# Optimization experiments

Measured on AMD Instinct MI355X. Metric: run time of the kernel, lower is better.

The kernel has to match this reference:

```python
import jax, jax.numpy as jnp
import numpy as np
from jax import lax

B, T, H, L, LAT, OUT, NH = 4096, 60, 512, 2, 128, 14, 4
EPS = 1e-5


def _ln(x, g, b):
    m = x.mean(-1, keepdims=True)
    v = ((x - m) ** 2).mean(-1, keepdims=True)
    return (x - m) / jnp.sqrt(v + EPS) * g + b


def setup_inputs() -> dict:
    key = jax.random.key(0)
    ks = jax.random.split(key, 24)
    f32 = jnp.float32
    def rn(k, shape, s=0.05):
        return jax.random.normal(k, shape, dtype=f32) * s
    return {
        'x': jax.random.normal(ks[0], (B, T, 17), dtype=f32),
        'conv1_w': rn(ks[1], (24, 9, 3)), 'conv1_b': rn(ks[2], (24,)),
        'bn1_g': jnp.ones(24, f32), 'bn1_b': jnp.zeros(24, f32),
        'bn1_rm': rn(ks[3], (24,), 0.1), 'bn1_rv': jnp.full((24,), 0.8, f32),
        'comp_w': rn(ks[4], (20, 8)), 'comp_b': rn(ks[5], (20,)),
        'proj_w': rn(ks[6], (H, 44)), 'proj_b': rn(ks[7], (H,)),
        'gates_w': rn(ks[8], (L, 5, H, 2 * H), 0.02), 'gates_b': rn(ks[9], (L, 5, H)),
        'retention': jnp.full((L, H), 0.9, f32),
        'expln_g': jnp.ones((L, H), f32), 'expln_b': jnp.zeros((L, H), f32),
        'ln_g': jnp.ones((L, H), f32), 'ln_b': jnp.zeros((L, H), f32),
        'attn_in_w': rn(ks[10], (3 * H, H), 0.02), 'attn_in_b': rn(ks[11], (3 * H,)),
        'attn_out_w': rn(ks[12], (H, H), 0.02), 'attn_out_b': rn(ks[13], (H,)),
        'bneck_w': rn(ks[14], (LAT, H)), 'bneck_b': rn(ks[15], (LAT,)),
        'bn2_g': jnp.ones(LAT, f32), 'bn2_b': jnp.zeros(LAT, f32),
        'bn2_rm': rn(ks[16], (LAT,), 0.1), 'bn2_rv': jnp.full((LAT,), 0.9, f32),
        'out_w': rn(ks[17], (OUT, LAT)), 'out_b': rn(ks[18], (OUT,)),
    }


def _forward(x, conv1_w, conv1_b, bn1_g, bn1_b, bn1_rm, bn1_rv, comp_w, comp_b,
             proj_w, proj_b, gates_w, gates_b, retention, expln_g, expln_b,
             ln_g, ln_b, attn_in_w, attn_in_b, attn_out_w, attn_out_b,
             bneck_w, bneck_b, bn2_g, bn2_b, bn2_rm, bn2_rv, out_w, out_b):
    bsz = x.shape[0]
    hd = proj_w.shape[0]
    nlayers = gates_w.shape[0]
    # --- conv branch on relative features (eval-mode BatchNorm) ---
    rel = x[:, :, :9].transpose(0, 2, 1)                      # [B,9,T]
    y = lax.conv_general_dilated(rel, conv1_w, (1,), [(1, 1)],
                                 dimension_numbers=('NCH', 'OIH', 'NCH'))
    y = jax.nn.relu(y + conv1_b[None, :, None])
    y = (y - bn1_rm[None, :, None]) / jnp.sqrt(bn1_rv + EPS)[None, :, None] \
        * bn1_g[None, :, None] + bn1_b[None, :, None]
    th = y.shape[2] // 2
    y = y[:, :, :th * 2].reshape(bsz, 24, th, 2).max(-1)      # MaxPool1d(2)
    rel_feat = y.transpose(0, 2, 1)                           # [B,30,24]
    # --- company embedding branch ---
    comp = jax.nn.relu(x[:, :30, 9:] @ comp_w.T + comp_b)     # [B,30,20]
    combined = jnp.concatenate([rel_feat, comp], -1) @ proj_w.T + proj_b  # [B,30,H]
    # --- stacked xLSTM over time ---
    h0 = jnp.zeros((nlayers, bsz, hd), x.dtype)
    c0 = jnp.zeros((nlayers, bsz, hd), x.dtype)
    def step(carry, x_t):
        h, c = carry
        inp = x_t
        hs, cs = [], []
        for l in range(nlayers):
            comb = jnp.concatenate([inp, h[l]], -1)           # [B,2H]
            g = jnp.einsum('bk,ghk->gbh', comb, gates_w[l]) + gates_b[l][:, None, :]
            f = jax.nn.sigmoid(g[0]); i = jax.nn.sigmoid(g[1])
            o = jax.nn.sigmoid(g[2]); cc = jnp.tanh(g[3]); m = jax.nn.sigmoid(g[4])
            r = retention[l]
            c_new = f * c[l] + i * cc
            c_new = c_new * r + (1 - r) * c[l]
            c_new = m * c_new + (1 - m) * c[l]
            o_exp = jax.nn.sigmoid(_ln(o, expln_g[l], expln_b[l]))  # exp(z)/(1+exp(z))
            h_new = _ln(o_exp * jnp.tanh(c_new), ln_g[l], ln_b[l])
            hs.append(h_new); cs.append(c_new)
            inp = h_new
        return (jnp.stack(hs), jnp.stack(cs)), inp
    _, seq = lax.scan(step, (h0, c0), combined.transpose(1, 0, 2))
    seq = seq.transpose(1, 0, 2)                              # [B,30,H]
    # --- multi-head self attention (eval, 4 heads) ---
    dh = hd // NH
    qkv = seq @ attn_in_w.T + attn_in_b
    q, k, v = jnp.split(qkv, 3, axis=-1)
    q = q.reshape(bsz, -1, NH, dh); k = k.reshape(bsz, -1, NH, dh); v = v.reshape(bsz, -1, NH, dh)
    scores = jnp.einsum('bqhd,bkhd->bhqk', q, k) / jnp.sqrt(jnp.float32(dh))
    attn = jnp.einsum('bhqk,bkhd->bqhd', jax.nn.softmax(scores, -1), v)
    attn = attn.reshape(bsz, -1, hd) @ attn_out_w.T + attn_out_b
    final = attn[:, -1, :]
    latent = final @ bneck_w.T + bneck_b
    latent = (latent - bn2_rm) / jnp.sqrt(bn2_rv + EPS) * bn2_g + bn2_b
    return latent @ out_w.T + out_b


def reference(x, conv1_w, conv1_b, bn1_g, bn1_b, bn1_rm, bn1_rv, comp_w, comp_b,
              proj_w, proj_b, gates_w, gates_b, retention, expln_g, expln_b,
              ln_g, ln_b, attn_in_w, attn_in_b, attn_out_w, attn_out_b,
              bneck_w, bneck_b, bn2_g, bn2_b, bn2_rm, bn2_rv, out_w, out_b):
    return _forward(x, conv1_w, conv1_b, bn1_g, bn1_b, bn1_rm, bn1_rv, comp_w, comp_b,
                    proj_w, proj_b, gates_w, gates_b, retention, expln_g, expln_b,
                    ln_g, ln_b, attn_in_w, attn_in_b, attn_out_w, attn_out_b,
                    bneck_w, bneck_b, bn2_g, bn2_b, bn2_rm, bn2_rv, out_w, out_b)
```

## Files before the change

kernel.cpp:

```cpp
#include <hip/hip_runtime.h>
#include <hip/hip_bf16.h>

#define B_   4096
#define T_   60
#define TT   30
#define H_   512
#define L_   2
#define NH_  4
#define DH_  128
#define LAT_ 128
#define OUT_ 14
#define NGATE_ (5*H_)
#define EPSF 1e-5f
#define FEATK 64
#define K0M  (FEATK + H_)

typedef __attribute__((ext_vector_type(8))) short bf16x8;
typedef __attribute__((ext_vector_type(4))) float f32x4;

__device__ __forceinline__ float sigmoidf_(float x) { return 1.0f / (1.0f + __expf(-x)); }
__device__ __forceinline__ float bf2f(short s) {
    return __uint_as_float(((unsigned)(unsigned short)s) << 16);
}

__device__ __forceinline__ void async_load16(const void* g, void* l) {
    __builtin_amdgcn_global_load_lds((const __attribute__((address_space(1))) void*)g,
                                     (__attribute__((address_space(3))) void*)l, 16, 0, 0);
}

__global__ __launch_bounds__(256) void cvt_bf16(const float* __restrict__ in,
                                                __hip_bfloat16* __restrict__ out, long n) {
    long i = (long)blockIdx.x * blockDim.x + threadIdx.x;
    long stride = (long)gridDim.x * blockDim.x;
    for (; i < n; i += stride) out[i] = __float2bfloat16(in[i]);
}

__global__ __launch_bounds__(256) void zero_f32(float* __restrict__ p, long n) {
    long i = (long)blockIdx.x * blockDim.x + threadIdx.x;
    long stride = (long)gridDim.x * blockDim.x;
    for (; i < n; i += stride) p[i] = 0.0f;
}

__global__ __launch_bounds__(256)
void build_w0m(const float* __restrict__ gw, const float* __restrict__ pw,
               const float* __restrict__ pb, const float* __restrict__ gb,
               __hip_bfloat16* __restrict__ w0m, float* __restrict__ bc) {
    const int tid = threadIdx.x;
    const int n = blockIdx.x * 4 + (tid >> 6);
    const int f = tid & 63;
    const float* wrow = gw + (long)n * (2 * H_);
    float acc = 0.f;
    if (f < 44) {
        for (int k = 0; k < H_; ++k) acc += wrow[k] * pw[k * 44 + f];
    }
    w0m[(long)n * K0M + f] = __float2bfloat16(acc);
    #pragma unroll
    for (int j = 0; j < 8; ++j) {
        int col = f * 8 + j;
        w0m[(long)n * K0M + FEATK + col] = __float2bfloat16(wrow[H_ + col]);
    }
    float s = 0.f;
    #pragma unroll
    for (int j = 0; j < 8; ++j) s += wrow[f * 8 + j] * pb[f * 8 + j];
    #pragma unroll
    for (int off = 32; off > 0; off >>= 1) s += __shfl_down(s, off, 64);
    if (f == 0) bc[n] = gb[n] + s;
}

__global__ __launch_bounds__(256)
void build_wkd(const float* __restrict__ aiw, __hip_bfloat16* __restrict__ wkd) {
    int i = blockIdx.x * 256 + threadIdx.x;
    if (i >= 2048 * 512) return;
    int n = i >> 9, k = i & 511;
    float v = ((k >> 7) == (n >> 9)) ? aiw[(H_ + k) * H_ + (n & 511)] : 0.f;
    wkd[i] = __float2bfloat16(v);
}

__global__ __launch_bounds__(256)
void build_wvd(const float* __restrict__ aiw, __hip_bfloat16* __restrict__ wvd) {
    int i = blockIdx.x * 256 + threadIdx.x;
    if (i >= 512 * 2048) return;
    int n = i >> 11, k = i & 2047;
    float v = ((k >> 9) == (n >> 7)) ? aiw[(2 * H_ + n) * H_ + (k & 511)] : 0.f;
    wvd[i] = __float2bfloat16(v);
}

__global__ __launch_bounds__(256)
void frontend_kernel(const float* __restrict__ x,
                     const float* __restrict__ cw, const float* __restrict__ cb,
                     const float* __restrict__ bg, const float* __restrict__ bb,
                     const float* __restrict__ brm, const float* __restrict__ brv,
                     const float* __restrict__ compw, const float* __restrict__ compb,
                     __hip_bfloat16* __restrict__ feat_out) {
    const int b = blockIdx.x, tid = threadIdx.x;
    __shared__ float xs[T_ * 17];
    __shared__ float ybuf[24][T_];
    __shared__ float feat[TT][44];

    for (int i = tid; i < T_ * 17; i += 256) xs[i] = x[(long)b * T_ * 17 + i];
    __syncthreads();

    for (int i = tid; i < 24 * T_; i += 256) {
        int oc = i / T_, t = i % T_;
        float acc = cb[oc];
        #pragma unroll
        for (int kk = 0; kk < 3; ++kk) {
            int tt = t + kk - 1;
            if (tt >= 0 && tt < T_) {
                #pragma unroll
                for (int ic = 0; ic < 9; ++ic)
                    acc += xs[tt * 17 + ic] * cw[(oc * 9 + ic) * 3 + kk];
            }
        }
        acc = fmaxf(acc, 0.f);
        acc = (acc - brm[oc]) * rsqrtf(brv[oc] + EPSF) * bg[oc] + bb[oc];
        ybuf[oc][t] = acc;
    }
    __syncthreads();

    for (int i = tid; i < TT * 24; i += 256) {
        int u = i / 24, oc = i % 24;
        feat[u][oc] = fmaxf(ybuf[oc][2 * u], ybuf[oc][2 * u + 1]);
    }
    for (int i = tid; i < TT * 20; i += 256) {
        int u = i / 20, oc = i % 20;
        float acc = compb[oc];
        #pragma unroll
        for (int j = 0; j < 8; ++j) acc += xs[u * 17 + 9 + j] * compw[oc * 8 + j];
        feat[u][24 + oc] = fmaxf(acc, 0.f);
    }
    __syncthreads();

    for (int i = tid; i < TT * FEATK; i += 256) {
        int u = i >> 6, c = i & 63;
        float v = (c < 44) ? feat[u][c] : 0.f;
        feat_out[((long)b * TT + u) * FEATK + c] = __float2bfloat16(v);
    }
}

template <int WRITE_BF16>
__device__ __forceinline__
void gemm_core(const __hip_bfloat16* __restrict__ A0, int lda0,
               const __hip_bfloat16* __restrict__ A1, int lda1, int ksplit,
               const __hip_bfloat16* __restrict__ W, int ldw,
               const float* __restrict__ bias,
               void* __restrict__ Cout, int ldc, int K, int bx, int by) {
    __shared__ __hip_bfloat16 As[128 * 64];
    __shared__ __hip_bfloat16 Bs[128 * 64];
    const int tid = threadIdx.x;
    const int wave = tid >> 6, lane = tid & 63;
    const long m0 = (long)by * 128;
    const long n0 = (long)bx * 128;

    f32x4 acc[4][4] = {};

    for (int k0 = 0; k0 < K; k0 += 64) {
        __syncthreads();
        #pragma unroll
        for (int it = 0; it < 4; ++it) {
            int id = it * 256 + tid;
            int row = id >> 3;
            int kc = ((id & 7) ^ (row & 7)) << 3;
            int gk = k0 + kc;
            const __hip_bfloat16* srcA;
            if (gk < ksplit) srcA = A0 + (m0 + row) * (long)lda0 + gk;
            else             srcA = A1 + (m0 + row) * (long)lda1 + (gk - ksplit);
            async_load16(srcA, &As[id * 8]);
            const __hip_bfloat16* srcB = W + (n0 + row) * (long)ldw + gk;
            async_load16(srcB, &Bs[id * 8]);
        }
        __syncthreads();
        #pragma unroll
        for (int ks = 0; ks < 2; ++ks) {
            const int kb = ((ks * 4 + (lane >> 4)) ^ (lane & 7)) << 3;
            const int ar = (wave >> 1) * 64 + (lane & 15);
            const int br = (wave & 1) * 64 + (lane & 15);
            bf16x8 afr[4], bfr[4];
            #pragma unroll
            for (int i = 0; i < 4; ++i) afr[i] = *(const bf16x8*)&As[(ar + i * 16) * 64 + kb];
            #pragma unroll
            for (int i = 0; i < 4; ++i) bfr[i] = *(const bf16x8*)&Bs[(br + i * 16) * 64 + kb];
            #pragma unroll
            for (int mi = 0; mi < 4; ++mi)
                #pragma unroll
                for (int ni = 0; ni < 4; ++ni)
                    acc[mi][ni] = __builtin_amdgcn_mfma_f32_16x16x32_bf16(afr[mi], bfr[ni], acc[mi][ni], 0, 0, 0);
        }
    }

    const int cr = (lane >> 4) * 4;
    const int ccol = lane & 15;
    #pragma unroll
    for (int ni = 0; ni < 4; ++ni) {
        long col = n0 + (wave & 1) * 64 + ni * 16 + ccol;
        float bv = bias ? bias[col] : 0.f;
        #pragma unroll
        for (int mi = 0; mi < 4; ++mi) {
            long rowb = m0 + (wave >> 1) * 64 + mi * 16 + cr;
            #pragma unroll
            for (int r = 0; r < 4; ++r) {
                float v = acc[mi][ni][r] + bv;
                if (WRITE_BF16)
                    ((__hip_bfloat16*)Cout)[(rowb + r) * (long)ldc + col] = __float2bfloat16(v);
                else
                    ((float*)Cout)[(rowb + r) * (long)ldc + col] = v;
            }
        }
    }
}

template <int WRITE_BF16>
__global__ __launch_bounds__(256)
void gemm_bias(const __hip_bfloat16* __restrict__ A0, int lda0,
               const __hip_bfloat16* __restrict__ A1, int lda1, int ksplit,
               const __hip_bfloat16* __restrict__ W, int ldw,
               const float* __restrict__ bias,
               void* __restrict__ Cout, int ldc, int K) {
    gemm_core<WRITE_BF16>(A0, lda0, A1, lda1, ksplit, W, ldw, bias, Cout, ldc, K,
                          blockIdx.x, blockIdx.y);
}

template <int WRITE_BF16>
__global__ __launch_bounds__(256)
void gemm_dual_db(const __hip_bfloat16* A0a, int lda0a, const __hip_bfloat16* A1a,
                  int lda1a, int Ka, const __hip_bfloat16* Wa,
                  const float* biasa, void* Ca, int ksplita, int ldwa,
                  const __hip_bfloat16* A0b, int lda0b, const __hip_bfloat16* A1b,
                  int lda1b, int Kb, const __hip_bfloat16* Wb,
                  const float* biasb, void* Cb, int ksplitb, int ldwb,
                  int ldc) {
    const int id = blockIdx.x;
    const int xcd = id & 7;
    const int mhalf = xcd >> 2;
    const int czg = xcd & 3;
    const int rest = id >> 3;
    const int m = mhalf * 16 + (rest & 15);
    const int colz = czg * 10 + (rest >> 4);
    const int col = colz % 20;
    const int z = colz / 20;
    const __hip_bfloat16* A0 = z ? A0b : A0a;
    const __hip_bfloat16* A1 = z ? A1b : A1a;
    const __hip_bfloat16* W  = z ? Wb  : Wa;
    const float* bias        = z ? biasb : biasa;
    void* Cout               = z ? Cb : Ca;
    int lda0 = z ? lda0b : lda0a;
    int lda1 = z ? lda1b : lda1a;
    int K    = z ? Kb : Ka;
    int ksplit = z ? ksplitb : ksplita;
    int ldw    = z ? ldwb : ldwa;

    __shared__ __hip_bfloat16 As[2][128 * 32];
    __shared__ __hip_bfloat16 Bs[2][128 * 32];
    const int tid = threadIdx.x;
    const int wave = tid >> 6, lane = tid & 63;
    const long m0 = (long)m * 128;
    const long n0 = (long)col * 128;

    f32x4 acc[4][4] = {};

    auto stage = [&](int hb, int k0) {
        #pragma unroll
        for (int it = 0; it < 2; ++it) {
            int sid = it * 256 + tid;
            int row = sid >> 2;
            int kc = ((sid & 3) ^ ((row >> 1) & 3)) << 3;
            int gk = k0 + kc;
            const __hip_bfloat16* srcA;
            if (gk < ksplit) srcA = A0 + (m0 + row) * (long)lda0 + gk;
            else             srcA = A1 + (m0 + row) * (long)lda1 + (gk - ksplit);
            async_load16(srcA, &As[hb][sid * 8]);
            const __hip_bfloat16* srcB = W + (n0 + row) * (long)ldw + gk;
            async_load16(srcB, &Bs[hb][sid * 8]);
        }
    };

    stage(0, 0);
    const int nslab = K >> 5;
    const int kb = ((lane >> 4) ^ ((lane >> 1) & 3)) << 3;
    const int ar = (wave >> 1) * 64 + (lane & 15);
    const int br = (wave & 1) * 64 + (lane & 15);

    for (int kk = 0; kk < nslab; ++kk) {
        const int hb = kk & 1;
        __syncthreads();
        if (kk + 1 < nslab) stage(hb ^ 1, (kk + 1) << 5);
        bf16x8 afr[4], bfr[4];
        #pragma unroll
        for (int i = 0; i < 4; ++i) afr[i] = *(const bf16x8*)&As[hb][(ar + i * 16) * 32 + kb];
        #pragma unroll
        for (int i = 0; i < 4; ++i) bfr[i] = *(const bf16x8*)&Bs[hb][(br + i * 16) * 32 + kb];
        #pragma unroll
        for (int mi = 0; mi < 4; ++mi)
            #pragma unroll
            for (int ni = 0; ni < 4; ++ni)
                acc[mi][ni] = __builtin_amdgcn_mfma_f32_16x16x32_bf16(afr[mi], bfr[ni], acc[mi][ni], 0, 0, 0);
    }

    const int cr = (lane >> 4) * 4;
    const int ccol = lane & 15;
    #pragma unroll
    for (int ni = 0; ni < 4; ++ni) {
        long ccol2 = n0 + (wave & 1) * 64 + ni * 16 + ccol;
        float bv = bias ? bias[ccol2] : 0.f;
        #pragma unroll
        for (int mi = 0; mi < 4; ++mi) {
            long rowb = m0 + (wave >> 1) * 64 + mi * 16 + cr;
            #pragma unroll
            for (int r = 0; r < 4; ++r) {
                float v = acc[mi][ni][r] + bv;
                if (WRITE_BF16)
                    ((__hip_bfloat16*)Cout)[(rowb + r) * (long)ldc + ccol2] = __float2bfloat16(v);
                else
                    ((float*)Cout)[(rowb + r) * (long)ldc + ccol2] = v;
            }
        }
    }
}

__device__ __forceinline__ void block_reduce2(float& a, float& b, float* red) {
    #pragma unroll
    for (int off = 32; off > 0; off >>= 1) {
        a += __shfl_down(a, off, 64);
        b += __shfl_down(b, off, 64);
    }
    int lane = threadIdx.x & 63, w = threadIdx.x >> 6;
    if (lane == 0) { red[w] = a; red[8 + w] = b; }
    __syncthreads();
    a = red[0] + red[1] + red[2] + red[3];
    b = red[8] + red[9] + red[10] + red[11];
    __syncthreads();
}

__device__ __forceinline__
void gate_ew_body(const __hip_bfloat16* __restrict__ g, float* __restrict__ c,
                  const float* __restrict__ ret,
                  const float* __restrict__ elg, const float* __restrict__ elb,
                  const float* __restrict__ lng, const float* __restrict__ lnb,
                  __hip_bfloat16* __restrict__ hout, long hstride, int b) {
    const int tid = threadIdx.x;
    const __hip_bfloat16* gr = g + (long)b * NGATE_;
    __shared__ float red[16];

    float o_[2], cn_[2];
    float s = 0.f, s2 = 0.f;
    #pragma unroll
    for (int u = 0; u < 2; ++u) {
        int j = tid + u * 256;
        float fg = __bfloat162float(gr[j]);
        float ig = __bfloat162float(gr[512 + j]);
        float og = __bfloat162float(gr[1024 + j]);
        float cg = __bfloat162float(gr[1536 + j]);
        float mg = __bfloat162float(gr[2048 + j]);
        float f = sigmoidf_(fg), i = sigmoidf_(ig), o = sigmoidf_(og);
        float cc = tanhf(cg), m = sigmoidf_(mg);
        float cold = c[(long)b * H_ + j];
        float r = ret[j];
        float cn = f * cold + i * cc;
        cn = cn * r + (1.f - r) * cold;
        cn = m * cn + (1.f - m) * cold;
        c[(long)b * H_ + j] = cn;
        o_[u] = o; cn_[u] = cn;
        s += o; s2 += o * o;
    }
    block_reduce2(s, s2, red);
    float mean = s * (1.f / H_);
    float var = s2 * (1.f / H_) - mean * mean;
    float rstd = rsqrtf(var + EPSF);

    float val[2];
    float s3 = 0.f, s4 = 0.f;
    #pragma unroll
    for (int u = 0; u < 2; ++u) {
        int j = tid + u * 256;
        float on = (o_[u] - mean) * rstd * elg[j] + elb[j];
        float oe = sigmoidf_(on);
        float v = oe * tanhf(cn_[u]);
        val[u] = v; s3 += v; s4 += v * v;
    }
    block_reduce2(s3, s4, red);
    float mean2 = s3 * (1.f / H_);
    float var2 = s4 * (1.f / H_) - mean2 * mean2;
    float rstd2 = rsqrtf(var2 + EPSF);
    #pragma unroll
    for (int u = 0; u < 2; ++u) {
        int j = tid + u * 256;
        float h = (val[u] - mean2) * rstd2 * lng[j] + lnb[j];
        hout[(long)b * hstride + j] = __float2bfloat16(h);
    }
}

__global__ __launch_bounds__(256)
void gate_ew(const __hip_bfloat16* __restrict__ g, float* __restrict__ c,
             const float* __restrict__ ret,
             const float* __restrict__ elg, const float* __restrict__ elb,
             const float* __restrict__ lng, const float* __restrict__ lnb,
             __hip_bfloat16* __restrict__ hout, long hstride) {
    gate_ew_body(g, c, ret, elg, elb, lng, lnb, hout, hstride, blockIdx.x);
}

__global__ __launch_bounds__(256)
void gate_ew_dual(const __hip_bfloat16* ga, float* ca, const float* reta,
                  const float* elga, const float* elba,
                  const float* lnga, const float* lnba,
                  __hip_bfloat16* houta, long hstridea,
                  const __hip_bfloat16* gb, float* cb, const float* retb,
                  const float* elgb, const float* elbb,
                  const float* lngb, const float* lnbb,
                  __hip_bfloat16* houtb, long hstrideb) {
    int bid = blockIdx.x;
    bool isB = bid >= B_;
    int b = isB ? bid - B_ : bid;
    const __hip_bfloat16* g = isB ? gb : ga;
    float* c        = isB ? cb : ca;
    const float* ret = isB ? retb : reta;
    const float* elg = isB ? elgb : elga;
    const float* elb = isB ? elbb : elba;
    const float* lng = isB ? lngb : lnga;
    const float* lnb = isB ? lnbb : lnba;
    __hip_bfloat16* hout = isB ? houtb : houta;
    long hstride = isB ? hstrideb : hstridea;
    gate_ew_body(g, c, ret, elg, elb, lng, lnb, hout, hstride, b);
}

__global__ __launch_bounds__(256)
void attn_fused(const __hip_bfloat16* __restrict__ seq,
                const __hip_bfloat16* __restrict__ U,
                __hip_bfloat16* __restrict__ sbar) {
    const int b = blockIdx.x, tid = threadIdx.x;
    const int h = tid >> 6, lane = tid & 63;
    const int c0 = lane * 8;
    __shared__ float ps[NH_ * TT];
    const float scale = 0.08838834764831845f;

    float uq[8];
    {
        bf16x8 uv = *(const bf16x8*)&U[(size_t)b * (NH_ * H_) + h * H_ + c0];
        for (int j = 0; j < 8; ++j) uq[j] = bf2f(uv[j]);
    }
    const __hip_bfloat16* srow = seq + (size_t)b * TT * H_;

    for (int t = 0; t < TT; ++t) {
        bf16x8 sv = *(const bf16x8*)&srow[t * H_ + c0];
        float a = 0.f;
        for (int j = 0; j < 8; ++j) a += uq[j] * bf2f(sv[j]);
        a += __shfl_xor(a, 32);
        a += __shfl_xor(a, 16);
        a += __shfl_xor(a, 8);
        a += __shfl_xor(a, 4);
        a += __shfl_xor(a, 2);
        a += __shfl_xor(a, 1);
        if (lane == 0) ps[h * TT + t] = a * scale;
    }
    __syncthreads();

    float mx = -1e30f;
    for (int t = 0; t < TT; ++t) mx = fmaxf(mx, ps[h * TT + t]);
    float den = 0.f;
    for (int t = 0; t < TT; ++t) den += __expf(ps[h * TT + t] - mx);
    float inv = 1.f / den;

    float accv[8];
    for (int j = 0; j < 8; ++j) accv[j] = 0.f;
    for (int t = 0; t < TT; ++t) {
        float w = __expf(ps[h * TT + t] - mx) * inv;
        bf16x8 sv = *(const bf16x8*)&srow[t * H_ + c0];
        for (int j = 0; j < 8; ++j) accv[j] += w * bf2f(sv[j]);
    }
    bf16x8 outv;
    for (int j = 0; j < 8; ++j) {
        __hip_bfloat16 hv = __float2bfloat16(accv[j]);
        outv[j] = *(short*)&hv;
    }
    *(bf16x8*)&sbar[(size_t)b * (NH_ * H_) + h * H_ + c0] = outv;
}

__global__ __launch_bounds__(128)
void head_kernel(const float* __restrict__ lat_in,
                 const float* __restrict__ g2, const float* __restrict__ b2,
                 const float* __restrict__ rm2, const float* __restrict__ rv2,
                 const float* __restrict__ ow, const float* __restrict__ ob,
                 float* __restrict__ out) {
    const int b = blockIdx.x, tid = threadIdx.x;
    __shared__ float ls[LAT_];
    float a = lat_in[(long)b * LAT_ + tid];
    ls[tid] = (a - rm2[tid]) * rsqrtf(rv2[tid] + EPSF) * g2[tid] + b2[tid];
    __syncthreads();
    if (tid < OUT_) {
        float acc = ob[tid];
        #pragma unroll 4
        for (int j = 0; j < LAT_; ++j) acc += ls[j] * ow[tid * LAT_ + j];
        out[(long)b * OUT_ + tid] = acc;
    }
}

extern "C" void kernel_launch(void* const* d_in, const int* in_sizes, int n_in,
                              void* d_out, int out_size, void* d_ws, size_t ws_size,
                              hipStream_t stream) {
    const float* x        = (const float*)d_in[0];
    const float* conv1_w  = (const float*)d_in[1];
    const float* conv1_b  = (const float*)d_in[2];
    const float* bn1_g    = (const float*)d_in[3];
    const float* bn1_b    = (const float*)d_in[4];
    const float* bn1_rm   = (const float*)d_in[5];
    const float* bn1_rv   = (const float*)d_in[6];
    const float* comp_w   = (const float*)d_in[7];
    const float* comp_b   = (const float*)d_in[8];
    const float* proj_w   = (const float*)d_in[9];
    const float* proj_b   = (const float*)d_in[10];
    const float* gates_w  = (const float*)d_in[11];
    const float* gates_b  = (const float*)d_in[12];
    const float* retention= (const float*)d_in[13];
    const float* expln_g  = (const float*)d_in[14];
    const float* expln_b  = (const float*)d_in[15];
    const float* ln_g     = (const float*)d_in[16];
    const float* ln_b     = (const float*)d_in[17];
    const float* attn_in_w  = (const float*)d_in[18];
    const float* attn_in_b  = (const float*)d_in[19];
    const float* attn_out_w = (const float*)d_in[20];
    const float* attn_out_b = (const float*)d_in[21];
    const float* bneck_w  = (const float*)d_in[22];
    const float* bneck_b  = (const float*)d_in[23];
    const float* bn2_g    = (const float*)d_in[24];
    const float* bn2_b    = (const float*)d_in[25];
    const float* bn2_rm   = (const float*)d_in[26];
    const float* bn2_rv   = (const float*)d_in[27];
    const float* out_w    = (const float*)d_in[28];
    const float* out_b    = (const float*)d_in[29];
    float* out = (float*)d_out;

    char* base = (char*)d_ws;
    size_t off = 0;
    auto alloc = [&](size_t nbytes) -> char* {
        char* p = base + off;
        off += (nbytes + 255) & ~(size_t)255;
        return p;
    };
    __hip_bfloat16* seq_bf = (__hip_bfloat16*)alloc((size_t)B_ * TT * H_ * 2);
    size_t g_bytes = (size_t)B_ * NGATE_ * 2;
    char* un = alloc(2 * g_bytes);
    __hip_bfloat16* gA_bf   = (__hip_bfloat16*)un;
    __hip_bfloat16* gB_bf   = (__hip_bfloat16*)(un + g_bytes);
    __hip_bfloat16* U_bf    = (__hip_bfloat16*)un;
    __hip_bfloat16* sbar_bf = (__hip_bfloat16*)(un + (size_t)16 * 1024 * 1024);
    __hip_bfloat16* wkd_bf  = (__hip_bfloat16*)(un + (size_t)32 * 1024 * 1024);
    __hip_bfloat16* wvd_bf  = (__hip_bfloat16*)(un + (size_t)35 * 1024 * 1024);
    __hip_bfloat16* feat_bf = (__hip_bfloat16*)alloc((size_t)B_ * TT * FEATK * 2);
    float*          c0    = (float*)alloc((size_t)B_ * H_ * 4);
    float*          c1    = (float*)alloc((size_t)B_ * H_ * 4);
    __hip_bfloat16* h0_bf = (__hip_bfloat16*)alloc((size_t)B_ * H_ * 2);
    __hip_bfloat16* q_bf  = (__hip_bfloat16*)alloc((size_t)B_ * H_ * 2);
    __hip_bfloat16* fin_bf = q_bf;
    __hip_bfloat16* av_bf = (__hip_bfloat16*)alloc((size_t)B_ * H_ * 2);
    float*          lat_f = (float*)alloc((size_t)B_ * LAT_ * 4);
    __hip_bfloat16* gw_bf = (__hip_bfloat16*)alloc((size_t)L_ * 5 * H_ * 2 * H_ * 2);
    __hip_bfloat16* w0m_bf = (__hip_bfloat16*)alloc((size_t)NGATE_ * K0M * 2);
    float*          bc_f  = (float*)alloc((size_t)NGATE_ * 4);
    __hip_bfloat16* ai_bf = (__hip_bfloat16*)alloc((size_t)H_ * H_ * 2);
    __hip_bfloat16* ao_bf = (__hip_bfloat16*)alloc((size_t)H_ * H_ * 2);
    __hip_bfloat16* bw_bf = (__hip_bfloat16*)alloc((size_t)LAT_ * H_ * 2);
    (void)ws_size; (void)in_sizes; (void)n_in; (void)out_size;

    const int WL = 5 * H_ * 2 * H_;
    cvt_bf16<<<1024, 256, 0, stream>>>(gates_w + WL, gw_bf + WL, (long)WL);
    build_w0m<<<NGATE_ / 4, 256, 0, stream>>>(gates_w, proj_w, proj_b, gates_b,
                                              w0m_bf, bc_f);
    cvt_bf16<<<256, 256, 0, stream>>>(attn_in_w, ai_bf, (long)H_ * H_);
    cvt_bf16<<<256, 256, 0, stream>>>(attn_out_w, ao_bf, (long)H_ * H_);
    cvt_bf16<<<64, 256, 0, stream>>>(bneck_w, bw_bf, (long)LAT_ * H_);
    zero_f32<<<2048, 256, 0, stream>>>(c0, (long)2 * B_ * H_);

    frontend_kernel<<<B_, 256, 0, stream>>>(x, conv1_w, conv1_b, bn1_g, bn1_b, bn1_rm,
                                            bn1_rv, comp_w, comp_b, feat_bf);

    const dim3 ggrid(NGATE_ / 128, B_ / 128);

    gemm_bias<1><<<ggrid, 256, 0, stream>>>(
        feat_bf, TT * FEATK, (const __hip_bfloat16*)nullptr, 0, FEATK,
        w0m_bf, K0M, bc_f, (void*)gB_bf, NGATE_, FEATK);
    gate_ew<<<B_, 256, 0, stream>>>(gB_bf, c0, retention, expln_g, expln_b,
                                    ln_g, ln_b, h0_bf, H_);

    for (int t = 0; t < TT - 1; ++t) {
        gemm_dual_db<1><<<1280, 256, 0, stream>>>(
            h0_bf, H_, (t == 0) ? (const __hip_bfloat16*)nullptr
                                : seq_bf + (size_t)(t - 1) * H_,
            TT * H_, (t == 0) ? H_ : 2 * H_, gw_bf + WL, gates_b + NGATE_, (void*)gA_bf,
            H_, 2 * H_,
            feat_bf + (size_t)(t + 1) * FEATK, TT * FEATK, h0_bf, H_, K0M,
            w0m_bf, bc_f, (void*)gB_bf,
            FEATK, K0M,
            NGATE_);
        gate_ew_dual<<<2 * B_, 256, 0, stream>>>(
            gA_bf, c1, retention + H_, expln_g + H_, expln_b + H_,
            ln_g + H_, ln_b + H_, seq_bf + (size_t)t * H_, TT * H_,
            gB_bf, c0, retention, expln_g, expln_b,
            ln_g, ln_b, h0_bf, H_);
    }
    gemm_bias<1><<<ggrid, 256, 0, stream>>>(
        h0_bf, H_, seq_bf + (size_t)(TT - 2) * H_, TT * H_, H_,
        gw_bf + WL, 2 * H_, gates_b + NGATE_, (void*)gA_bf, NGATE_, 2 * H_);
    gate_ew<<<B_, 256, 0, stream>>>(gA_bf, c1, retention + H_, expln_g + H_,
                                    expln_b + H_, ln_g + H_, ln_b + H_,
                                    seq_bf + (size_t)(TT - 1) * H_, TT * H_);

    build_wkd<<<4096, 256, 0, stream>>>(attn_in_w, wkd_bf);
    build_wvd<<<4096, 256, 0, stream>>>(attn_in_w, wvd_bf);

    gemm_bias<1><<<dim3(H_ / 128, B_ / 128), 256, 0, stream>>>(
        seq_bf + (size_t)29 * H_, TT * H_, (const __hip_bfloat16*)nullptr, 0, H_,
        ai_bf, H_, attn_in_b, (void*)q_bf, H_, H_);

    gemm_bias<1><<<dim3(2048 / 128, B_ / 128), 256, 0, stream>>>(
        q_bf, H_, (const __hip_bfloat16*)nullptr, 0, H_,
        wkd_bf, H_, (const float*)nullptr, (void*)U_bf, 2048, H_);

    attn_fused<<<B_, 256, 0, stream>>>(seq_bf, U_bf, sbar_bf);

    gemm_bias<1><<<dim3(H_ / 128, B_ / 128), 256, 0, stream>>>(
        sbar_bf, 2048, (const __hip_bfloat16*)nullptr, 0, 2048,
        wvd_bf, 2048, attn_in_b + 2 * H_, (void*)av_bf, H_, 2048);

    gemm_bias<1><<<dim3(H_ / 128, B_ / 128), 256, 0, stream>>>(
        av_bf, H_, (const __hip_bfloat16*)nullptr, 0, H_,
        ao_bf, H_, attn_out_b, (void*)fin_bf, H_, H_);

    gemm_bias<0><<<dim3(LAT_ / 128, B_ / 128), 256, 0, stream>>>(
        fin_bf, H_, (const __hip_bfloat16*)nullptr, 0, H_,
        bw_bf, H_, bneck_b, (void*)lat_f, LAT_, H_);
    head_kernel<<<B_, 128, 0, stream>>>(lat_f, bn2_g, bn2_b, bn2_rm, bn2_rv,
                                        out_w, out_b, out);
}
```

Baseline: 2.755 ms.

## Fuse gate nonlinearities and cell update into the recurrent gate GEMM epilogue

Result: faster. 2.666 ms (-3.2%).

```diff
diff --git a/kernel.cpp b/kernel.cpp
--- a/kernel.cpp
+++ b/kernel.cpp
@@ -16,6 +16,7 @@
 #define K0M  (FEATK + H_)
 
 typedef __attribute__((ext_vector_type(8))) short bf16x8;
+typedef __attribute__((ext_vector_type(4))) short bf16x4;
 typedef __attribute__((ext_vector_type(4))) float f32x4;
 
 __device__ __forceinline__ float sigmoidf_(float x) { return 1.0f / (1.0f + __expf(-x)); }
@@ -26,6 +27,11 @@
 __device__ __forceinline__ void async_load16(const void* g, void* l) {
     __builtin_amdgcn_global_load_lds((const __attribute__((address_space(1))) void*)g,
                                      (__attribute__((address_space(3))) void*)l, 16, 0, 0);
+}
+
+__device__ __forceinline__ int perm_row(int n) {
+    int g = n >> 9, j = n & 511;
+    return (j >> 4) * 80 + g * 16 + (j & 15);
 }
 
 __global__ __launch_bounds__(256) void cvt_bf16(const float* __restrict__ in,
@@ -42,22 +48,31 @@
 }
 
 __global__ __launch_bounds__(256)
+void perm_w1(const float* __restrict__ gw, __hip_bfloat16* __restrict__ w1p) {
+    long i = (long)blockIdx.x * 256 + threadIdx.x;
+    if (i >= (long)NGATE_ * 2 * H_) return;
+    int n = (int)(i >> 10), k = (int)(i & 1023);
+    w1p[(long)perm_row(n) * (2 * H_) + k] = __float2bfloat16(gw[i]);
+}
+
+__global__ __launch_bounds__(256)
 void build_w0m(const float* __restrict__ gw, const float* __restrict__ pw,
                const float* __restrict__ pb, const float* __restrict__ gb,
-               __hip_bfloat16* __restrict__ w0m, float* __restrict__ bc) {
+               __hip_bfloat16* __restrict__ w0p, float* __restrict__ bc) {
     const int tid = threadIdx.x;
     const int n = blockIdx.x * 4 + (tid >> 6);
     const int f = tid & 63;
+    const long np = perm_row(n);
     const float* wrow = gw + (long)n * (2 * H_);
     float acc = 0.f;
     if (f < 44) {
         for (int k = 0; k < H_; ++k) acc += wrow[k] * pw[k * 44 + f];
     }
-    w0m[(long)n * K0M + f] = __float2bfloat16(acc);
+    w0p[np * K0M + f] = __float2bfloat16(acc);
     #pragma unroll
     for (int j = 0; j < 8; ++j) {
         int col = f * 8 + j;
-        w0m[(long)n * K0M + FEATK + col] = __float2bfloat16(wrow[H_ + col]);
+        w0p[np * K0M + FEATK + col] = __float2bfloat16(wrow[H_ + col]);
     }
     float s = 0.f;
     #pragma unroll
@@ -220,43 +235,26 @@
                           blockIdx.x, blockIdx.y);
 }
 
-template <int WRITE_BF16>
-__global__ __launch_bounds__(256)
-void gemm_dual_db(const __hip_bfloat16* A0a, int lda0a, const __hip_bfloat16* A1a,
-                  int lda1a, int Ka, const __hip_bfloat16* Wa,
-                  const float* biasa, void* Ca, int ksplita, int ldwa,
-                  const __hip_bfloat16* A0b, int lda0b, const __hip_bfloat16* A1b,
-                  int lda1b, int Kb, const __hip_bfloat16* Wb,
-                  const float* biasb, void* Cb, int ksplitb, int ldwb,
-                  int ldc) {
-    const int id = blockIdx.x;
-    const int xcd = id & 7;
-    const int mhalf = xcd >> 2;
-    const int czg = xcd & 3;
-    const int rest = id >> 3;
-    const int m = mhalf * 16 + (rest & 15);
-    const int colz = czg * 10 + (rest >> 4);
-    const int col = colz % 20;
-    const int z = colz / 20;
-    const __hip_bfloat16* A0 = z ? A0b : A0a;
-    const __hip_bfloat16* A1 = z ? A1b : A1a;
-    const __hip_bfloat16* W  = z ? Wb  : Wa;
-    const float* bias        = z ? biasb : biasa;
-    void* Cout               = z ? Cb : Ca;
-    int lda0 = z ? lda0b : lda0a;
-    int lda1 = z ? lda1b : lda1a;
-    int K    = z ? Kb : Ka;
-    int ksplit = z ? ksplitb : ksplita;
-    int ldw    = z ? ldwb : ldwa;
-
+__device__ __forceinline__
+void fused_gate_core(const __hip_bfloat16* __restrict__ A0, int lda0,
+                     const __hip_bfloat16* __restrict__ A1, int lda1,
+                     int ksplit, int K,
+                     const __hip_bfloat16* __restrict__ Wp, int ldw,
+                     const float* __restrict__ bias,
+                     const float* __restrict__ ret,
+                     float* __restrict__ c_t,
+                     float* __restrict__ opre,
+                     float* __restrict__ tcn,
+                     int m, int nblk) {
     __shared__ __hip_bfloat16 As[2][128 * 32];
-    __shared__ __hip_bfloat16 Bs[2][128 * 32];
+    __shared__ __hip_bfloat16 Bs[2][80 * 32];
     const int tid = threadIdx.x;
     const int wave = tid >> 6, lane = tid & 63;
     const long m0 = (long)m * 128;
-    const long n0 = (long)col * 128;
-
-    f32x4 acc[4][4] = {};
+    const int n0row = nblk * 80;
+    const int jbase = nblk * 16;
+
+    f32x4 acc[2][5] = {};
 
     auto stage = [&](int hb, int k0) {
         #pragma unroll
@@ -269,52 +267,108 @@
             if (gk < ksplit) srcA = A0 + (m0 + row) * (long)lda0 + gk;
             else             srcA = A1 + (m0 + row) * (long)lda1 + (gk - ksplit);
             async_load16(srcA, &As[hb][sid * 8]);
-            const __hip_bfloat16* srcB = W + (n0 + row) * (long)ldw + gk;
-            async_load16(srcB, &Bs[hb][sid * 8]);
+        }
+        {
+            int sid = tid;
+            int row = sid >> 2;
+            int kc = ((sid & 3) ^ ((row >> 1) & 3)) << 3;
+            async_load16(Wp + (long)(n0row + row) * ldw + k0 + kc, &Bs[hb][sid * 8]);
+        }
+        if (tid < 64) {
+            int sid = 256 + tid;
+            int row = sid >> 2;
+            int kc = ((sid & 3) ^ ((row >> 1) & 3)) << 3;
+            async_load16(Wp + (long)(n0row + row) * ldw + k0 + kc, &Bs[hb][sid * 8]);
         }
     };
 
     stage(0, 0);
     const int nslab = K >> 5;
     const int kb = ((lane >> 4) ^ ((lane >> 1) & 3)) << 3;
-    const int ar = (wave >> 1) * 64 + (lane & 15);
-    const int br = (wave & 1) * 64 + (lane & 15);
+    const int arb = wave * 32 + (lane & 15);
+    const int brb = lane & 15;
 
     for (int kk = 0; kk < nslab; ++kk) {
         const int hb = kk & 1;
         __syncthreads();
         if (kk + 1 < nslab) stage(hb ^ 1, (kk + 1) << 5);
-        bf16x8 afr[4], bfr[4];
-        #pragma unroll
-        for (int i = 0; i < 4; ++i) afr[i] = *(const bf16x8*)&As[hb][(ar + i * 16) * 32 + kb];
-        #pragma unroll
-        for (int i = 0; i < 4; ++i) bfr[i] = *(const bf16x8*)&Bs[hb][(br + i * 16) * 32 + kb];
-        #pragma unroll
-        for (int mi = 0; mi < 4; ++mi)
+        bf16x8 afr[2], bfr[5];
+        #pragma unroll
+        for (int i = 0; i < 2; ++i) afr[i] = *(const bf16x8*)&As[hb][(arb + i * 16) * 32 + kb];
+        #pragma unroll
+        for (int i = 0; i < 5; ++i) bfr[i] = *(const bf16x8*)&Bs[hb][(brb + i * 16) * 32 + kb];
+        #pragma unroll
+        for (int mi = 0; mi < 2; ++mi)
             #pragma unroll
-            for (int ni = 0; ni < 4; ++ni)
-                acc[mi][ni] = __builtin_amdgcn_mfma_f32_16x16x32_bf16(afr[mi], bfr[ni], acc[mi][ni], 0, 0, 0);
-    }
-
-    const int cr = (lane >> 4) * 4;
-    const int ccol = lane & 15;
-    #pragma unroll
-    for (int ni = 0; ni < 4; ++ni) {
-        long ccol2 = n0 + (wave & 1) * 64 + ni * 16 + ccol;
-        float bv = bias ? bias[ccol2] : 0.f;
-        #pragma unroll
-        for (int mi = 0; mi < 4; ++mi) {
-            long rowb = m0 + (wave >> 1) * 64 + mi * 16 + cr;
-            #pragma unroll
-            for (int r = 0; r < 4; ++r) {
-                float v = acc[mi][ni][r] + bv;
-                if (WRITE_BF16)
-                    ((__hip_bfloat16*)Cout)[(rowb + r) * (long)ldc + ccol2] = __float2bfloat16(v);
-                else
-                    ((float*)Cout)[(rowb + r) * (long)ldc + ccol2] = v;
-            }
-        }
-    }
+            for (int ni = 0; ni < 5; ++ni)
+                acc[mi][ni] = __builtin_amdgcn_mfma_f32_16x16x32_bf16(bfr[ni], afr[mi], acc[mi][ni], 0, 0, 0);
+    }
+
+    const int q = lane >> 4;
+    #pragma unroll
+    for (int mi = 0; mi < 2; ++mi) {
+        const long b = m0 + wave * 32 + mi * 16 + (lane & 15);
+        f32x4 ov, tv;
+        #pragma unroll
+        for (int r = 0; r < 4; ++r) {
+            const int jg = jbase + 4 * q + r;
+            float f  = sigmoidf_(acc[mi][0][r] + bias[jg]);
+            float ii = sigmoidf_(acc[mi][1][r] + bias[512 + jg]);
+            float o  = sigmoidf_(acc[mi][2][r] + bias[1024 + jg]);
+            float cc = tanhf(acc[mi][3][r] + bias[1536 + jg]);
+            float mg = sigmoidf_(acc[mi][4][r] + bias[2048 + jg]);
+            float cold = c_t[(long)jg * B_ + b];
+            float rr = ret[jg];
+            float cn = f * cold + ii * cc;
+            cn = cn * rr + (1.f - rr) * cold;
+            cn = mg * cn + (1.f - mg) * cold;
+            c_t[(long)jg * B_ + b] = cn;
+            ov[r] = o;
+            tv[r] = tanhf(cn);
+        }
+        *(f32x4*)&opre[b * H_ + jbase + 4 * q] = ov;
+        *(f32x4*)&tcn [b * H_ + jbase + 4 * q] = tv;
+    }
+}
+
+__global__ __launch_bounds__(256)
+void fused_gate_single(const __hip_bfloat16* A0, int lda0, const __hip_bfloat16* A1,
+                       int lda1, int ksplit, int K,
+                       const __hip_bfloat16* Wp, int ldw,
+                       const float* bias, const float* ret, float* c_t,
+                       float* opre, float* tcn) {
+    const int id = blockIdx.x;
+    const int xcd = id & 7;
+    const int rest = id >> 3;
+    const int m = xcd * 4 + (rest & 3);
+    const int n = (rest >> 2) & 31;
+    fused_gate_core(A0, lda0, A1, lda1, ksplit, K, Wp, ldw, bias, ret, c_t,
+                    opre, tcn, m, n);
+}
+
+__global__ __launch_bounds__(256)
+void fused_gate_dual(const __hip_bfloat16* A0a, int lda0a, const __hip_bfloat16* A1a,
+                     int lda1a, int ksplita, int Ka,
+                     const __hip_bfloat16* Wpa, int ldwa,
+                     const float* biasa, const float* reta, float* cta,
+                     float* oprea, float* tcna,
+                     const __hip_bfloat16* A0b, int lda0b, const __hip_bfloat16* A1b,
+                     int lda1b, int ksplitb, int Kb,
+                     const __hip_bfloat16* Wpb, int ldwb,
+                     const float* biasb, const float* retb, float* ctb,
+                     float* opreb, float* tcnb) {
+    const int id = blockIdx.x;
+    const int xcd = id & 7;
+    const int rest = id >> 3;
+    const int m = xcd * 4 + (rest & 3);
+    const int n = (rest >> 2) & 31;
+    const int z = rest >> 7;
+    if (z == 0)
+        fused_gate_core(A0a, lda0a, A1a, lda1a, ksplita, Ka, Wpa, ldwa,
+                        biasa, reta, cta, oprea, tcna, m, n);
+    else
+        fused_gate_core(A0b, lda0b, A1b, lda1b, ksplitb, Kb, Wpb, ldwb,
+                        biasb, retb, ctb, opreb, tcnb, m, n);
 }
 
 __device__ __forceinline__ void block_reduce2(float& a, float& b, float* red) {
@@ -332,34 +386,22 @@
 }
 
 __device__ __forceinline__
-void gate_ew_body(const __hip_bfloat16* __restrict__ g, float* __restrict__ c,
-                  const float* __restrict__ ret,
+void gate_ln_body(const float* __restrict__ opre,
+                  const float* __restrict__ tcn,
                   const float* __restrict__ elg, const float* __restrict__ elb,
                   const float* __restrict__ lng, const float* __restrict__ lnb,
                   __hip_bfloat16* __restrict__ hout, long hstride, int b) {
     const int tid = threadIdx.x;
-    const __hip_bfloat16* gr = g + (long)b * NGATE_;
     __shared__ float red[16];
 
-    float o_[2], cn_[2];
+    float o_[2], t_[2];
     float s = 0.f, s2 = 0.f;
     #pragma unroll
     for (int u = 0; u < 2; ++u) {
         int j = tid + u * 256;
-        float fg = __bfloat162float(gr[j]);
-        float ig = __bfloat162float(gr[512 + j]);
-        float og = __bfloat162float(gr[1024 + j]);
-        float cg = __bfloat162float(gr[1536 + j]);
-        float mg = __bfloat162float(gr[2048 + j]);
-        float f = sigmoidf_(fg), i = sigmoidf_(ig), o = sigmoidf_(og);
-        float cc = tanhf(cg), m = sigmoidf_(mg);
-        float cold = c[(long)b * H_ + j];
-        float r = ret[j];
-        float cn = f * cold + i * cc;
-        cn = cn * r + (1.f - r) * cold;
-        cn = m * cn + (1.f - m) * cold;
-        c[(long)b * H_ + j] = cn;
-        o_[u] = o; cn_[u] = cn;
+        float o = opre[(long)b * H_ + j];
+        float t = tcn[(long)b * H_ + j];
+        o_[u] = o; t_[u] = t;
         s += o; s2 += o * o;
     }
     block_reduce2(s, s2, red);
@@ -373,8 +415,7 @@
     for (int u = 0; u < 2; ++u) {
         int j = tid + u * 256;
         float on = (o_[u] - mean) * rstd * elg[j] + elb[j];
-        float oe = sigmoidf_(on);
-        float v = oe * tanhf(cn_[u]);
+        float v = sigmoidf_(on) * t_[u];
         val[u] = v; s3 += v; s4 += v * v;
     }
     block_reduce2(s3, s4, red);
@@ -390,36 +431,30 @@
 }
 
 __global__ __launch_bounds__(256)
-void gate_ew(const __hip_bfloat16* __restrict__ g, float* __restrict__ c,
-             const float* __restrict__ ret,
+void gate_ln(const float* __restrict__ opre,
+             const float* __restrict__ tcn,
              const float* __restrict__ elg, const float* __restrict__ elb,
              const float* __restrict__ lng, const float* __restrict__ lnb,
              __hip_bfloat16* __restrict__ hout, long hstride) {
-    gate_ew_body(g, c, ret, elg, elb, lng, lnb, hout, hstride, blockIdx.x);
-}
-
-__global__ __launch_bounds__(256)
-void gate_ew_dual(const __hip_bfloat16* ga, float* ca, const float* reta,
+    gate_ln_body(opre, tcn, elg, elb, lng, lnb, hout, hstride, blockIdx.x);
+}
+
+__global__ __launch_bounds__(256)
+void gate_ln_dual(const float* oa, const float* ta,
                   const float* elga, const float* elba,
                   const float* lnga, const float* lnba,
                   __hip_bfloat16* houta, long hstridea,
-                  const __hip_bfloat16* gb, float* cb, const float* retb,
+                  const float* ob, const float* tb,
                   const float* elgb, const float* elbb,
                   const float* lngb, const float* lnbb,
                   __hip_bfloat16* houtb, long hstrideb) {
     int bid = blockIdx.x;
     bool isB = bid >= B_;
     int b = isB ? bid - B_ : bid;
-    const __hip_bfloat16* g = isB ? gb : ga;
-    float* c        = isB ? cb : ca;
-    const float* ret = isB ? retb : reta;
-    const float* elg = isB ? elgb : elga;
-    const float* elb = isB ? elbb : elba;
-    const float* lng = isB ? lngb : lnga;
-    const float* lnb = isB ? lnbb : lnba;
-    __hip_bfloat16* hout = isB ? houtb : houta;
-    long hstride = isB ? hstrideb : hstridea;
-    gate_ew_body(g, c, ret, elg, elb, lng, lnb, hout, hstride, b);
+    gate_ln_body(isB ? ob : oa, isB ? tb : ta,
+                 isB ? elgb : elga, isB ? elbb : elba,
+                 isB ? lngb : lnga, isB ? lnbb : lnba,
+                 isB ? houtb : houta, isB ? hstrideb : hstridea, b);
 }
 
 __global__ __launch_bounds__(256)
@@ -538,22 +573,24 @@
     __hip_bfloat16* seq_bf = (__hip_bfloat16*)alloc((size_t)B_ * TT * H_ * 2);
     size_t g_bytes = (size_t)B_ * NGATE_ * 2;
     char* un = alloc(2 * g_bytes);
-    __hip_bfloat16* gA_bf   = (__hip_bfloat16*)un;
-    __hip_bfloat16* gB_bf   = (__hip_bfloat16*)(un + g_bytes);
+    float* opreA = (float*)un;
+    float* tcnA  = (float*)(un + (size_t)8 * 1024 * 1024);
+    float* opreB = (float*)(un + (size_t)16 * 1024 * 1024);
+    float* tcnB  = (float*)(un + (size_t)24 * 1024 * 1024);
     __hip_bfloat16* U_bf    = (__hip_bfloat16*)un;
     __hip_bfloat16* sbar_bf = (__hip_bfloat16*)(un + (size_t)16 * 1024 * 1024);
     __hip_bfloat16* wkd_bf  = (__hip_bfloat16*)(un + (size_t)32 * 1024 * 1024);
     __hip_bfloat16* wvd_bf  = (__hip_bfloat16*)(un + (size_t)35 * 1024 * 1024);
     __hip_bfloat16* feat_bf = (__hip_bfloat16*)alloc((size_t)B_ * TT * FEATK * 2);
-    float*          c0    = (float*)alloc((size_t)B_ * H_ * 4);
-    float*          c1    = (float*)alloc((size_t)B_ * H_ * 4);
+    float*          c0t   = (float*)alloc((size_t)B_ * H_ * 4);
+    float*          c1t   = (float*)alloc((size_t)B_ * H_ * 4);
     __hip_bfloat16* h0_bf = (__hip_bfloat16*)alloc((size_t)B_ * H_ * 2);
     __hip_bfloat16* q_bf  = (__hip_bfloat16*)alloc((size_t)B_ * H_ * 2);
     __hip_bfloat16* fin_bf = q_bf;
     __hip_bfloat16* av_bf = (__hip_bfloat16*)alloc((size_t)B_ * H_ * 2);
     float*          lat_f = (float*)alloc((size_t)B_ * LAT_ * 4);
-    __hip_bfloat16* gw_bf = (__hip_bfloat16*)alloc((size_t)L_ * 5 * H_ * 2 * H_ * 2);
-    __hip_bfloat16* w0m_bf = (__hip_bfloat16*)alloc((size_t)NGATE_ * K0M * 2);
+    __hip_bfloat16* w1p_bf = (__hip_bfloat16*)alloc((size_t)NGATE_ * 2 * H_ * 2);
+    __hip_bfloat16* w0p_bf = (__hip_bfloat16*)alloc((size_t)NGATE_ * K0M * 2);
     float*          bc_f  = (float*)alloc((size_t)NGATE_ * 4);
     __hip_bfloat16* ai_bf = (__hip_bfloat16*)alloc((size_t)H_ * H_ * 2);
     __hip_bfloat16* ao_bf = (__hip_bfloat16*)alloc((size_t)H_ * H_ * 2);
@@ -561,46 +598,41 @@
     (void)ws_size; (void)in_sizes; (void)n_in; (void)out_size;
 
     const int WL = 5 * H_ * 2 * H_;
-    cvt_bf16<<<1024, 256, 0, stream>>>(gates_w + WL, gw_bf + WL, (long)WL);
+    perm_w1<<<(NGATE_ * 2 * H_) / 256, 256, 0, stream>>>(gates_w + WL, w1p_bf);
     build_w0m<<<NGATE_ / 4, 256, 0, stream>>>(gates_w, proj_w, proj_b, gates_b,
-                                              w0m_bf, bc_f);
+                                              w0p_bf, bc_f);
     cvt_bf16<<<256, 256, 0, stream>>>(attn_in_w, ai_bf, (long)H_ * H_);
     cvt_bf16<<<256, 256, 0, stream>>>(attn_out_w, ao_bf, (long)H_ * H_);
     cvt_bf16<<<64, 256, 0, stream>>>(bneck_w, bw_bf, (long)LAT_ * H_);
-    zero_f32<<<2048, 256, 0, stream>>>(c0, (long)2 * B_ * H_);
+    zero_f32<<<2048, 256, 0, stream>>>(c0t, (long)2 * B_ * H_);
 
     frontend_kernel<<<B_, 256, 0, stream>>>(x, conv1_w, conv1_b, bn1_g, bn1_b, bn1_rm,
                                             bn1_rv, comp_w, comp_b, feat_bf);
 
-    const dim3 ggrid(NGATE_ / 128, B_ / 128);
-
-    gemm_bias<1><<<ggrid, 256, 0, stream>>>(
-        feat_bf, TT * FEATK, (const __hip_bfloat16*)nullptr, 0, FEATK,
-        w0m_bf, K0M, bc_f, (void*)gB_bf, NGATE_, FEATK);
-    gate_ew<<<B_, 256, 0, stream>>>(gB_bf, c0, retention, expln_g, expln_b,
+    fused_gate_single<<<1024, 256, 0, stream>>>(
+        feat_bf, TT * FEATK, (const __hip_bfloat16*)nullptr, 0, FEATK, FEATK,
+        w0p_bf, K0M, bc_f, retention, c0t, opreB, tcnB);
+    gate_ln<<<B_, 256, 0, stream>>>(opreB, tcnB, expln_g, expln_b,
                                     ln_g, ln_b, h0_bf, H_);
 
     for (int t = 0; t < TT - 1; ++t) {
-        gemm_dual_db<1><<<1280, 256, 0, stream>>>(
+        fused_gate_dual<<<2048, 256, 0, stream>>>(
             h0_bf, H_, (t == 0) ? (const __hip_bfloat16*)nullptr
                                 : seq_bf + (size_t)(t - 1) * H_,
-            TT * H_, (t == 0) ? H_ : 2 * H_, gw_bf + WL, gates_b + NGATE_, (void*)gA_bf,
-            H_, 2 * H_,
-            feat_bf + (size_t)(t + 1) * FEATK, TT * FEATK, h0_bf, H_, K0M,
-            w0m_bf, bc_f, (void*)gB_bf,
-            FEATK, K0M,
-            NGATE_);
-        gate_ew_dual<<<2 * B_, 256, 0, stream>>>(
-            gA_bf, c1, retention + H_, expln_g + H_, expln_b + H_,
-            ln_g + H_, ln_b + H_, seq_bf + (size_t)t * H_, TT * H_,
-            gB_bf, c0, retention, expln_g, expln_b,
-            ln_g, ln_b, h0_bf, H_);
-    }
-    gemm_bias<1><<<ggrid, 256, 0, stream>>>(
-        h0_bf, H_, seq_bf + (size_t)(TT - 2) * H_, TT * H_, H_,
-        gw_bf + WL, 2 * H_, gates_b + NGATE_, (void*)gA_bf, NGATE_, 2 * H_);
-    gate_ew<<<B_, 256, 0, stream>>>(gA_bf, c1, retention + H_, expln_g + H_,
-                                    expln_b + H_, ln_g + H_, ln_b + H_,
+            TT * H_, H_, (t == 0) ? H_ : 2 * H_,
+            w1p_bf, 2 * H_, gates_b + NGATE_, retention + H_, c1t, opreA, tcnA,
+            feat_bf + (size_t)(t + 1) * FEATK, TT * FEATK, h0_bf, H_, FEATK, K0M,
+            w0p_bf, K0M, bc_f, retention, c0t, opreB, tcnB);
+        gate_ln_dual<<<2 * B_, 256, 0, stream>>>(
+            opreA, tcnA, expln_g + H_, expln_b + H_, ln_g + H_, ln_b + H_,
+            seq_bf + (size_t)t * H_, TT * H_,
+            opreB, tcnB, expln_g, expln_b, ln_g, ln_b, h0_bf, H_);
+    }
+    fused_gate_single<<<1024, 256, 0, stream>>>(
+        h0_bf, H_, seq_bf + (size_t)(TT - 2) * H_, TT * H_, H_, 2 * H_,
+        w1p_bf, 2 * H_, gates_b + NGATE_, retention + H_, c1t, opreA, tcnA);
+    gate_ln<<<B_, 256, 0, stream>>>(opreA, tcnA, expln_g + H_, expln_b + H_,
+                                    ln_g + H_, ln_b + H_,
                                     seq_bf + (size_t)(TT - 1) * H_, TT * H_);
 
     build_wkd<<<4096, 256, 0, stream>>>(attn_in_w, wkd_bf);
```
